# Kernel tuning notes

Hardware: AMD Instinct MI355X
Metric: run time of the kernel (lower is better)

Reference implementation:

```python
import jax, jax.numpy as jnp
import numpy as np

N, D = 12288, 64


def _ggc(x, adj, W, wih, whh, bih, bhh):
    # Gated graph conv, num_layers=1 (PyG semantics):
    #   m = adj @ (x @ W); x' = GRUCell(m, x)
    m = adj @ (x @ W)                      # [N, D]
    gi = m @ wih.T + bih                   # [N, 3D]
    gh = x @ whh.T + bhh                   # [N, 3D]
    i_r, i_z, i_n = jnp.split(gi, 3, axis=-1)
    h_r, h_z, h_n = jnp.split(gh, 3, axis=-1)
    r = jax.nn.sigmoid(i_r + h_r)
    z = jax.nn.sigmoid(i_z + h_z)
    n = jnp.tanh(i_n + r * h_n)
    return (1.0 - z) * n + z * x


def setup_inputs() -> dict:
    key = jax.random.key(0)
    ks = jax.random.split(key, 8)
    s = 1.0 / np.sqrt(D)
    return {
        "x": jax.random.normal(ks[0], (N, D), jnp.float32),
        "adj": jax.random.uniform(ks[1], (N, N), jnp.float32),
        "W1": jax.random.normal(ks[2], (D, D), jnp.float32) * s,
        "wih1": jax.random.normal(ks[3], (3 * D, D), jnp.float32) * s,
        "whh1": jax.random.normal(ks[4], (3 * D, D), jnp.float32) * s,
        "bih1": jnp.zeros((3 * D,), jnp.float32),
        "bhh1": jnp.zeros((3 * D,), jnp.float32),
        "W2": jax.random.normal(ks[5], (D, D), jnp.float32) * s,
        "wih2": jax.random.normal(ks[6], (3 * D, D), jnp.float32) * s,
        "whh2": jax.random.normal(ks[7], (3 * D, D), jnp.float32) * s,
        "bih2": jnp.zeros((3 * D,), jnp.float32),
        "bhh2": jnp.zeros((3 * D,), jnp.float32),
    }


def reference(x, adj, W1, wih1, whh1, bih1, bhh1, W2, wih2, whh2, bih2, bhh2):
    h = jax.nn.relu(_ggc(x, adj, W1, wih1, whh1, bih1, bhh1))
    # dropout is a no-op in eval mode (training=False)
    return jax.nn.relu(_ggc(h, adj, W2, wih2, whh2, bih2, bhh2))
```

## Files before the change

### kernel.cpp

```cpp
#include <hip/hip_runtime.h>
#include <hip/hip_bf16.h>
#include <cstdint>

#define NN 12288

typedef __attribute__((ext_vector_type(8))) short bfrag8;
typedef __attribute__((ext_vector_type(4))) float f32x4;
typedef __attribute__((ext_vector_type(4))) uint16_t u16x4;
typedef __attribute__((ext_vector_type(8))) uint16_t u16x8;

__device__ __forceinline__ uint16_t f2bf_rtn(float f) {
    uint32_t u = __float_as_uint(f);
    return (uint16_t)((u + 0x7fffu + ((u >> 16) & 1u)) >> 16);
}
__device__ __forceinline__ void split_bf(float f, uint16_t& hb, uint16_t& lb) {
    uint32_t u = __float_as_uint(f);
    hb = (uint16_t)(u >> 16);
    float fr = f - __uint_as_float(u & 0xffff0000u);
    lb = f2bf_rtn(fr);
}

__device__ __forceinline__ void lds_sync() {
    asm volatile("s_waitcnt lgkmcnt(0)" ::: "memory");
    __builtin_amdgcn_s_barrier();
    asm volatile("" ::: "memory");
}

__global__ void wt4_kernel(const float* __restrict__ w0, const float* __restrict__ w1,
                           const float* __restrict__ w2, const float* __restrict__ w3,
                           float* __restrict__ o0, float* __restrict__ o1,
                           float* __restrict__ o2, float* __restrict__ o3) {
    const float* w; float* o;
    switch (blockIdx.y) {
        case 0: w = w0; o = o0; break;
        case 1: w = w1; o = o1; break;
        case 2: w = w2; o = o2; break;
        default: w = w3; o = o3; break;
    }
    int i = blockIdx.x * 256 + threadIdx.x;
    if (i < 192 * 64) {
        int r = i / 64, k = i % 64;
        o[k * 192 + r] = w[i];
    }
}

__global__ void __launch_bounds__(256) xw_kernel(const float* __restrict__ X,
                                                 const float* __restrict__ W,
                                                 uint16_t* __restrict__ Bpk) {
    __shared__ __align__(16) float sW[64 * 65];
    __shared__ __align__(16) float sX[64 * 65];
    const int t = threadIdx.x;
    const int rb = blockIdx.x * 64;
    for (int i = t; i < 4096; i += 256) {
        int rr = i >> 6, cc = i & 63;
        sW[rr * 65 + cc] = W[i];
        sX[rr * 65 + cc] = X[(size_t)rb * 64 + i];
    }
    __syncthreads();
    const int r = t & 63;
    const int c0 = (t >> 6) * 16;
    float acc[16];
#pragma unroll
    for (int i = 0; i < 16; i++) acc[i] = 0.f;
    for (int k = 0; k < 64; k++) {
        float xv = sX[r * 65 + k];
#pragma unroll
        for (int i = 0; i < 16; i++) acc[i] += xv * sW[k * 65 + c0 + i];
    }
    const int j = rb + r;
    const size_t base = (size_t)(j >> 6) * 8192 + (size_t)((j >> 3) & 7) * 512 + (j & 7);
#pragma unroll
    for (int i = 0; i < 16; i++) {
        uint16_t hb, lb;
        split_bf(acc[i], hb, lb);
        size_t idx = base + (size_t)(c0 + i) * 8;
        Bpk[idx] = hb;
        Bpk[idx + 4096] = lb;
    }
}

__global__ void __launch_bounds__(256, 2) spmm_kernel(
    const float* __restrict__ adj,
    const uint16_t* __restrict__ Bpk,
    float* __restrict__ partial,
    int ktiles, int rev) {
    __shared__ __align__(16) uint16_t sAhi[4096];
    __shared__ __align__(16) uint16_t sAlo[4096];
    __shared__ __align__(16) uint16_t sB[8192];
    const int t = threadIdx.x;
    const int rb = blockIdx.x;
    const int kc = blockIdx.y;
    const int tile0 = kc * ktiles;
    const int wave = t >> 6, lane = t & 63;
    const int srow16 = t >> 4;
    const int skk = (t & 15) * 4;
    const float* aptr = adj + (size_t)rb * 64 * NN;
    const int arow = wave * 16 + (lane & 15);
    const int kq = lane >> 4;

    f32x4 acc[4];
#pragma unroll
    for (int i = 0; i < 4; i++) {
        acc[i][0] = 0.f; acc[i][1] = 0.f; acc[i][2] = 0.f; acc[i][3] = 0.f;
    }

    f32x4 lA0[4], lA1[4];
    u16x8 lB0[4], lB1[4];

    auto tid2glob = [&](int i) { return tile0 + (rev ? (ktiles - 1 - i) : i); };

    auto load_tile = [&](int tl, f32x4 (&lA)[4], u16x8 (&lB)[4]) {
        const float* ap = aptr + (size_t)tid2glob(tl) * 64;
#pragma unroll
        for (int it = 0; it < 4; ++it) {
            int row = it * 16 + srow16;
            lA[it] = *(const f32x4*)(ap + (size_t)row * NN + skk);
        }
        const u16x8* bsrc = (const u16x8*)(Bpk + (size_t)tid2glob(tl) * 8192);
#pragma unroll
        for (int i = 0; i < 4; ++i) lB[i] = bsrc[i * 256 + t];
    };

    auto stage_tile = [&](f32x4 (&lA)[4], u16x8 (&lB)[4]) {
#pragma unroll
        for (int it = 0; it < 4; ++it) {
            int row = it * 16 + srow16;
            u16x4 hi, lo;
#pragma unroll
            for (int q = 0; q < 4; q++) {
                uint16_t hb, lb;
                split_bf(lA[it][q], hb, lb);
                hi[q] = hb; lo[q] = lb;
            }
            int off = row * 128 + (((skk >> 3) ^ (row & 7)) << 4) + ((skk & 7) << 1);
            *(u16x4*)((char*)sAhi + off) = hi;
            *(u16x4*)((char*)sAlo + off) = lo;
        }
#pragma unroll
        for (int i = 0; i < 4; ++i) ((u16x8*)sB)[i * 256 + t] = lB[i];
    };

    auto compute_tile = [&]() {
#pragma unroll
        for (int ks = 0; ks < 2; ++ks) {
            const int chunk = ks * 4 + kq;
            const int aoff = arow * 128 + ((chunk ^ (arow & 7)) << 4);
            bfrag8 ahi = *(const bfrag8*)((const char*)sAhi + aoff);
            bfrag8 alo = *(const bfrag8*)((const char*)sAlo + aoff);
            const int bko = chunk * 512;
#pragma unroll
            for (int ct = 0; ct < 4; ++ct) {
                int col = ct * 16 + (lane & 15);
                bfrag8 bh = *(const bfrag8*)&sB[bko + col * 8];
                bfrag8 bl = *(const bfrag8*)&sB[4096 + bko + col * 8];
                acc[ct] = __builtin_amdgcn_mfma_f32_16x16x32_bf16(ahi, bh, acc[ct], 0, 0, 0);
                acc[ct] = __builtin_amdgcn_mfma_f32_16x16x32_bf16(alo, bh, acc[ct], 0, 0, 0);
                acc[ct] = __builtin_amdgcn_mfma_f32_16x16x32_bf16(ahi, bl, acc[ct], 0, 0, 0);
            }
        }
    };

    load_tile(0, lA0, lB0);
    load_tile(1, lA1, lB1);

    for (int tl = 0; tl < ktiles; tl += 2) {
        lds_sync();
        stage_tile(lA0, lB0);
        lds_sync();
        if (tl + 2 < ktiles) load_tile(tl + 2, lA0, lB0);
        compute_tile();
        lds_sync();
        stage_tile(lA1, lB1);
        lds_sync();
        if (tl + 3 < ktiles) load_tile(tl + 3, lA1, lB1);
        compute_tile();
    }

    float* pout = partial + (size_t)kc * ((size_t)NN * 64);
    const int orow = rb * 64 + wave * 16 + (lane >> 4) * 4;
    const int ocol = lane & 15;
#pragma unroll
    for (int ct = 0; ct < 4; ++ct) {
#pragma unroll
        for (int r = 0; r < 4; ++r) {
            pout[(size_t)(orow + r) * 64 + ct * 16 + ocol] = acc[ct][r];
        }
    }
}

__global__ void __launch_bounds__(256, 4) gru_kernel(
    const float* __restrict__ partial, int ksplit,
    const float* __restrict__ Xin,
    const float* __restrict__ wtih,
    const float* __restrict__ wthh,
    const float* __restrict__ bih,
    const float* __restrict__ bhh,
    float* __restrict__ hout) {
    __shared__ __align__(16) float sM[32 * 64];
    __shared__ __align__(16) float sX[32 * 64];
    const int t = threadIdx.x;
    const int nb = blockIdx.x * 32;
    {
        size_t g0 = (size_t)nb * 64 + (size_t)t * 8;
        f32x4 s0, s1;
        {
            const f32x4* p0 = (const f32x4*)(partial + g0);
            s0 = p0[0]; s1 = p0[1];
        }
        for (int p = 1; p < ksplit; p++) {
            const f32x4* pp = (const f32x4*)(partial + (size_t)p * ((size_t)NN * 64) + g0);
            f32x4 a = pp[0], b = pp[1];
#pragma unroll
            for (int q = 0; q < 4; q++) { s0[q] += a[q]; s1[q] += b[q]; }
        }
        *(f32x4*)&sM[t * 8] = s0;
        *(f32x4*)&sM[t * 8 + 4] = s1;
        const f32x4* px = (const f32x4*)(Xin + g0);
        *(f32x4*)&sX[t * 8] = px[0];
        *(f32x4*)&sX[t * 8 + 4] = px[1];
    }
    __syncthreads();
    const int wave = t >> 6, lane = t & 63;
    const int nodebase = wave * 8;
    float a_ir[8], a_iz[8], a_in[8], a_hr[8], a_hz[8], a_hn[8];
#pragma unroll
    for (int n = 0; n < 8; n++) {
        a_ir[n] = 0.f; a_iz[n] = 0.f; a_in[n] = 0.f;
        a_hr[n] = 0.f; a_hz[n] = 0.f; a_hn[n] = 0.f;
    }
    for (int k = 0; k < 64; k++) {
        float w0 = wtih[k * 192 + lane];
        float w1 = wtih[k * 192 + 64 + lane];
        float w2 = wtih[k * 192 + 128 + lane];
        float w3 = wthh[k * 192 + lane];
        float w4 = wthh[k * 192 + 64 + lane];
        float w5 = wthh[k * 192 + 128 + lane];
#pragma unroll
        for (int n = 0; n < 8; n++) {
            float mv = sM[(nodebase + n) * 64 + k];
            float xv = sX[(nodebase + n) * 64 + k];
            a_ir[n] += w0 * mv; a_iz[n] += w1 * mv; a_in[n] += w2 * mv;
            a_hr[n] += w3 * xv; a_hz[n] += w4 * xv; a_hn[n] += w5 * xv;
        }
    }
    const float b0 = bih[lane], b1 = bih[64 + lane], b2 = bih[128 + lane];
    const float b3 = bhh[lane], b4 = bhh[64 + lane], b5 = bhh[128 + lane];
#pragma unroll
    for (int n = 0; n < 8; n++) {
        float ir = a_ir[n] + b0, iz = a_iz[n] + b1, inn = a_in[n] + b2;
        float hr = a_hr[n] + b3, hz = a_hz[n] + b4, hn = a_hn[n] + b5;
        float r = 1.f / (1.f + __expf(-(ir + hr)));
        float z = 1.f / (1.f + __expf(-(iz + hz)));
        float nt = tanhf(inn + r * hn);
        float xv = sX[(nodebase + n) * 64 + lane];
        float o = (1.f - z) * nt + z * xv;
        o = fmaxf(o, 0.f);
        size_t oi = (size_t)(nb + nodebase + n) * 64 + lane;
        hout[oi] = o;
    }
}

extern "C" void kernel_launch(void* const* d_in, const int* in_sizes, int n_in,
                              void* d_out, int out_size, void* d_ws, size_t ws_size,
                              hipStream_t stream) {
    const float* x    = (const float*)d_in[0];
    const float* adj  = (const float*)d_in[1];
    const float* W1   = (const float*)d_in[2];
    const float* wih1 = (const float*)d_in[3];
    const float* whh1 = (const float*)d_in[4];
    const float* bih1 = (const float*)d_in[5];
    const float* bhh1 = (const float*)d_in[6];
    const float* W2   = (const float*)d_in[7];
    const float* wih2 = (const float*)d_in[8];
    const float* whh2 = (const float*)d_in[9];
    const float* bih2 = (const float*)d_in[10];
    const float* bhh2 = (const float*)d_in[11];
    float* out = (float*)d_out;

    char* p = (char*)d_ws;
    float* wtih1 = (float*)p; p += (size_t)192 * 64 * 4;
    float* wthh1 = (float*)p; p += (size_t)192 * 64 * 4;
    float* wtih2 = (float*)p; p += (size_t)192 * 64 * 4;
    float* wthh2 = (float*)p; p += (size_t)192 * 64 * 4;
    float* h     = (float*)p; p += (size_t)NN * 64 * 4;
    uint16_t* Bpk = (uint16_t*)p; p += (size_t)NN * 64 * 2 * 2;
    float* partial = (float*)p;
    size_t used = (size_t)(p - (char*)d_ws);
    size_t unit = (size_t)NN * 64 * 4;

    int ksplit = 1;
    const int opts[3] = {4, 2, 1};
    for (int i = 0; i < 3; i++) {
        if (used + (size_t)opts[i] * unit <= ws_size) { ksplit = opts[i]; break; }
    }
    int ktiles = 192 / ksplit;

    wt4_kernel<<<dim3(48, 4), 256, 0, stream>>>(wih1, whh1, wih2, whh2,
                                                wtih1, wthh1, wtih2, wthh2);

    xw_kernel<<<192, 256, 0, stream>>>(x, W1, Bpk);
    spmm_kernel<<<dim3(192, ksplit), 256, 0, stream>>>(adj, Bpk, partial, ktiles, 0);
    gru_kernel<<<384, 256, 0, stream>>>(partial, ksplit, x, wtih1, wthh1, bih1, bhh1, h);
    xw_kernel<<<192, 256, 0, stream>>>(h, W2, Bpk);
    spmm_kernel<<<dim3(192, ksplit), 256, 0, stream>>>(adj, Bpk, partial, ktiles, 1);
    gru_kernel<<<384, 256, 0, stream>>>(partial, ksplit, h, wtih2, wthh2, bih2, bhh2, out);
}
```

Baseline: 349.9 us.

## Load A fragments directly into registers and double-buffer B in LDS

```diff
diff --git a/kernel.cpp b/kernel.cpp
--- a/kernel.cpp
+++ b/kernel.cpp
@@ -84,19 +84,16 @@
     const uint16_t* __restrict__ Bpk,
     float* __restrict__ partial,
     int ktiles, int rev) {
-    __shared__ __align__(16) uint16_t sAhi[4096];
-    __shared__ __align__(16) uint16_t sAlo[4096];
-    __shared__ __align__(16) uint16_t sB[8192];
+    __shared__ __align__(16) uint16_t sB0[8192];
+    __shared__ __align__(16) uint16_t sB1[8192];
     const int t = threadIdx.x;
     const int rb = blockIdx.x;
     const int kc = blockIdx.y;
     const int tile0 = kc * ktiles;
     const int wave = t >> 6, lane = t & 63;
-    const int srow16 = t >> 4;
-    const int skk = (t & 15) * 4;
-    const float* aptr = adj + (size_t)rb * 64 * NN;
     const int arow = wave * 16 + (lane & 15);
     const int kq = lane >> 4;
+    const float* arp = adj + ((size_t)(rb * 64 + arow)) * NN;
 
     f32x4 acc[4];
 #pragma unroll
@@ -104,76 +101,77 @@
         acc[i][0] = 0.f; acc[i][1] = 0.f; acc[i][2] = 0.f; acc[i][3] = 0.f;
     }
 
-    f32x4 lA0[4], lA1[4];
-    u16x8 lB0[4], lB1[4];
-
     auto tid2glob = [&](int i) { return tile0 + (rev ? (ktiles - 1 - i) : i); };
 
-    auto load_tile = [&](int tl, f32x4 (&lA)[4], u16x8 (&lB)[4]) {
-        const float* ap = aptr + (size_t)tid2glob(tl) * 64;
-#pragma unroll
-        for (int it = 0; it < 4; ++it) {
-            int row = it * 16 + srow16;
-            lA[it] = *(const f32x4*)(ap + (size_t)row * NN + skk);
-        }
+    f32x4 aC[4], aN[4];
+    auto load_A = [&](int tl, f32x4 (&a)[4]) {
+        const float* p = arp + (size_t)tid2glob(tl) * 64 + kq * 8;
+        a[0] = *(const f32x4*)(p);
+        a[1] = *(const f32x4*)(p + 4);
+        a[2] = *(const f32x4*)(p + 32);
+        a[3] = *(const f32x4*)(p + 36);
+    };
+    bfrag8 ahi[2], alo[2];
+    auto conv_A = [&](f32x4 (&a)[4]) {
+#pragma unroll
+        for (int ks = 0; ks < 2; ++ks) {
+#pragma unroll
+            for (int h = 0; h < 2; ++h) {
+#pragma unroll
+                for (int q = 0; q < 4; ++q) {
+                    uint16_t hb, lb;
+                    split_bf(a[ks * 2 + h][q], hb, lb);
+                    ahi[ks][h * 4 + q] = (short)hb;
+                    alo[ks][h * 4 + q] = (short)lb;
+                }
+            }
+        }
+    };
+
+    u16x8 breg[4];
+    auto load_B = [&](int tl) {
         const u16x8* bsrc = (const u16x8*)(Bpk + (size_t)tid2glob(tl) * 8192);
 #pragma unroll
-        for (int i = 0; i < 4; ++i) lB[i] = bsrc[i * 256 + t];
-    };
-
-    auto stage_tile = [&](f32x4 (&lA)[4], u16x8 (&lB)[4]) {
-#pragma unroll
-        for (int it = 0; it < 4; ++it) {
-            int row = it * 16 + srow16;
-            u16x4 hi, lo;
-#pragma unroll
-            for (int q = 0; q < 4; q++) {
-                uint16_t hb, lb;
-                split_bf(lA[it][q], hb, lb);
-                hi[q] = hb; lo[q] = lb;
-            }
-            int off = row * 128 + (((skk >> 3) ^ (row & 7)) << 4) + ((skk & 7) << 1);
-            *(u16x4*)((char*)sAhi + off) = hi;
-            *(u16x4*)((char*)sAlo + off) = lo;
-        }
-#pragma unroll
-        for (int i = 0; i < 4; ++i) ((u16x8*)sB)[i * 256 + t] = lB[i];
-    };
-
-    auto compute_tile = [&]() {
+        for (int i = 0; i < 4; ++i) breg[i] = bsrc[i * 256 + t];
+    };
+    auto stage_B = [&](uint16_t* sB) {
+#pragma unroll
+        for (int i = 0; i < 4; ++i) ((u16x8*)sB)[i * 256 + t] = breg[i];
+    };
+
+    auto compute = [&](const uint16_t* sB) {
 #pragma unroll
         for (int ks = 0; ks < 2; ++ks) {
-            const int chunk = ks * 4 + kq;
-            const int aoff = arow * 128 + ((chunk ^ (arow & 7)) << 4);
-            bfrag8 ahi = *(const bfrag8*)((const char*)sAhi + aoff);
-            bfrag8 alo = *(const bfrag8*)((const char*)sAlo + aoff);
-            const int bko = chunk * 512;
+            const int bko = (ks * 4 + kq) * 512;
 #pragma unroll
             for (int ct = 0; ct < 4; ++ct) {
                 int col = ct * 16 + (lane & 15);
                 bfrag8 bh = *(const bfrag8*)&sB[bko + col * 8];
                 bfrag8 bl = *(const bfrag8*)&sB[4096 + bko + col * 8];
-                acc[ct] = __builtin_amdgcn_mfma_f32_16x16x32_bf16(ahi, bh, acc[ct], 0, 0, 0);
-                acc[ct] = __builtin_amdgcn_mfma_f32_16x16x32_bf16(alo, bh, acc[ct], 0, 0, 0);
-                acc[ct] = __builtin_amdgcn_mfma_f32_16x16x32_bf16(ahi, bl, acc[ct], 0, 0, 0);
+                acc[ct] = __builtin_amdgcn_mfma_f32_16x16x32_bf16(ahi[ks], bh, acc[ct], 0, 0, 0);
+                acc[ct] = __builtin_amdgcn_mfma_f32_16x16x32_bf16(alo[ks], bh, acc[ct], 0, 0, 0);
+                acc[ct] = __builtin_amdgcn_mfma_f32_16x16x32_bf16(ahi[ks], bl, acc[ct], 0, 0, 0);
             }
         }
     };
 
-    load_tile(0, lA0, lB0);
-    load_tile(1, lA1, lB1);
+    load_B(0);
+    load_A(0, aC);
+    load_A(1, aN);
 
     for (int tl = 0; tl < ktiles; tl += 2) {
+        stage_B(sB0);
+        if (tl + 1 < ktiles) load_B(tl + 1);
         lds_sync();
-        stage_tile(lA0, lB0);
+        conv_A(aC);
+        if (tl + 2 < ktiles) load_A(tl + 2, aC);
+        compute(sB0);
+        stage_B(sB1);
+        if (tl + 2 < ktiles) load_B(tl + 2);
         lds_sync();
-        if (tl + 2 < ktiles) load_tile(tl + 2, lA0, lB0);
-        compute_tile();
-        lds_sync();
-        stage_tile(lA1, lB1);
-        lds_sync();
-        if (tl + 3 < ktiles) load_tile(tl + 3, lA1, lB1);
-        compute_tile();
+        conv_A(aN);
+        if (tl + 3 < ktiles) load_A(tl + 3, aN);
+        compute(sB1);
     }
 
     float* pout = partial + (size_t)kc * ((size_t)NN * 64);
```

Result: slower. 370.1 us (+5.8%).
